# Kernel tuning notes

Hardware: AMD Instinct MI355X
Metric: run time of the kernel (lower is better)

## Reference

```python
import jax, jax.numpy as jnp
import numpy as np

BATCH = 8
HEADS = 16
Q_LEN = 1024
K_LEN = 1024
HEAD_DIM = 64


def setup_inputs() -> dict:
    key = jax.random.key(0)
    kq, kk, kv, kl = jax.random.split(key, 4)
    queries = jax.random.normal(kq, (BATCH * HEADS, Q_LEN, HEAD_DIM), dtype=jnp.float32)
    keys = jax.random.normal(kk, (BATCH * HEADS, K_LEN, HEAD_DIM), dtype=jnp.float32)
    values = jax.random.normal(kv, (BATCH * HEADS, K_LEN, HEAD_DIM), dtype=jnp.float32)
    valid_lens = jax.random.randint(kl, (BATCH,), 0, K_LEN, dtype=jnp.int64)
    return {"queries": queries, "keys": keys, "values": values, "valid_lens": valid_lens}


def reference(queries, keys, values, valid_lens):
    # queries/keys/values: [B*H, S, d]; valid_lens: [B] int
    bh, q_len, d = queries.shape
    k_len = keys.shape[1]
    b = valid_lens.shape[0]
    h = bh // b
    scale = 1.0 / float(d) ** 0.5
    # [B*H, q, k] scores
    scores = jnp.einsum("bqd,bkd->bqk", queries, keys) * scale
    # encode_mask: True where key position >= valid_len -> fill with -1e6
    mask = jnp.arange(k_len)[None, :] >= valid_lens[:, None]  # [B, k]
    scores = scores.reshape(b, h, q_len, k_len)
    scores = jnp.where(mask[:, None, None, :], jnp.float32(-1000000.0), scores)
    attn = jax.nn.softmax(scores, axis=-1)  # [B, H, q, k]
    out = jnp.einsum("bhqk,bhkd->bhqd", attn, values.reshape(b, h, k_len, d))
    return out.reshape(bh, q_len, d)
```

## Files before the change

kernel.cpp:

```cpp
#include <hip/hip_runtime.h>


#define H_PER_B 16
#define QL 1024
#define KL 1024
#define DH 64
#define KT 64
#define QW 16
#define NW 8
#define QB (QW * NW)
#define KST 72
#define VST 72
#define PST 68

typedef float  f32x4  __attribute__((ext_vector_type(4)));
typedef short  bf16x8 __attribute__((ext_vector_type(8)));
typedef short  bf16x4 __attribute__((ext_vector_type(4)));

__device__ __forceinline__ unsigned bfbits(float f) {
    unsigned u = __builtin_bit_cast(unsigned, f);
    u += 0x7FFFu + ((u >> 16) & 1u);
    return u >> 16;
}
__device__ __forceinline__ unsigned pk2(float a, float b) {
    return bfbits(a) | (bfbits(b) << 16);
}
__device__ __forceinline__ short s2bf(float f) {
    return (short)bfbits(f);
}

__global__ __launch_bounds__(512) void attn_fwd(
    const float* __restrict__ Q, const float* __restrict__ K,
    const float* __restrict__ V, const int* __restrict__ vlen_p,
    float* __restrict__ O)
{
    const int bh    = blockIdx.x;
    const int qtile = blockIdx.y;
    const int vlen  = vlen_p[bh / H_PER_B];

    const int tid  = threadIdx.x;
    const int wave = tid >> 6;
    const int lane = tid & 63;
    const int lg   = lane >> 4;
    const int lr   = lane & 15;

    const float* Qb = Q + ((size_t)bh * QL + (size_t)qtile * QB + (size_t)wave * QW) * DH;
    const float* Kb = K + (size_t)bh * KL * DH;
    const float* Vb = V + (size_t)bh * KL * DH;

    __shared__ short Ks [2][KT][KST];
    __shared__ short VsT[2][DH][VST];
    __shared__ short Ps [NW][QW][PST];

    const float QSCALE = 0.18033688011112042f;
    bf16x8 qf[2];
#pragma unroll
    for (int dc = 0; dc < 2; ++dc) {
        const float* p = Qb + (size_t)lr * DH + dc * 32 + 8 * lg;
        float4 a = *(const float4*)p;
        float4 b = *(const float4*)(p + 4);
        uint4 u;
        u.x = pk2(a.x * QSCALE, a.y * QSCALE);
        u.y = pk2(a.z * QSCALE, a.w * QSCALE);
        u.z = pk2(b.x * QSCALE, b.y * QSCALE);
        u.w = pk2(b.z * QSCALE, b.w * QSCALE);
        qf[dc] = __builtin_bit_cast(bf16x8, u);
    }

    f32x4 acc[4];
#pragma unroll
    for (int i = 0; i < 4; ++i) acc[i] = (f32x4){0.f, 0.f, 0.f, 0.f};
    float lsum[4] = {0.f, 0.f, 0.f, 0.f};

    const bool  all_masked = (vlen == 0);
    const float msel       = all_masked ? 1.0f : 0.0f;
    const int nt = all_masked ? (KL / KT) : ((vlen + KT - 1) >> 6);

    const int kr0 = tid >> 4;
    const int dc0 = (tid & 15) * 4;
    const int vd  = tid & 63;
    const int vk0 = (tid >> 6) * 8;
    const float* Vcol = Vb + vd;

    float4 ka[2];
    float  va[8];

#define LOADK(t)                                                              \
    {                                                                         \
        const float* kp = Kb + (size_t)((t) * KT) * DH;                       \
        ka[0] = *(const float4*)(kp + (size_t)kr0 * DH + dc0);                \
        ka[1] = *(const float4*)(kp + (size_t)(kr0 + 32) * DH + dc0);         \
    }
#define LOADV(t)                                                              \
    _Pragma("unroll")                                                         \
    for (int j = 0; j < 8; ++j)                                               \
        va[j] = Vcol[(size_t)((t) * KT + vk0 + j) * DH];
#define STOREKV(b)                                                            \
    {                                                                         \
        uint2 k0 = {pk2(ka[0].x, ka[0].y), pk2(ka[0].z, ka[0].w)};            \
        uint2 k1 = {pk2(ka[1].x, ka[1].y), pk2(ka[1].z, ka[1].w)};            \
        *(bf16x4*)&Ks[b][kr0][dc0]      = __builtin_bit_cast(bf16x4, k0);     \
        *(bf16x4*)&Ks[b][kr0 + 32][dc0] = __builtin_bit_cast(bf16x4, k1);     \
        uint4 vv = {pk2(va[0], va[1]), pk2(va[2], va[3]),                     \
                    pk2(va[4], va[5]), pk2(va[6], va[7])};                    \
        *(bf16x8*)&VsT[b][vd][vk0] = __builtin_bit_cast(bf16x8, vv);          \
    }

    LOADK(0); LOADV(0); STOREKV(0);

    for (int t = 0; t < nt; ++t) {
        const int buf = t & 1;
        __syncthreads();

        if (t + 1 < nt) { LOADK(t + 1); LOADV(t + 1); }
        const int kt0 = t * KT;

#pragma unroll
        for (int kh = 0; kh < 4; ++kh) {
            f32x4 c = (f32x4){0.f, 0.f, 0.f, 0.f};
#pragma unroll
            for (int dc = 0; dc < 2; ++dc) {
                bf16x8 kf = *(const bf16x8*)&Ks[buf][kh * 16 + lr][dc * 32 + 8 * lg];
                c = __builtin_amdgcn_mfma_f32_16x16x32_bf16(qf[dc], kf, c, 0, 0, 0);
            }
            const int  kpos   = kt0 + kh * 16 + lr;
            const bool masked = (kpos >= vlen);
#pragma unroll
            for (int r = 0; r < 4; ++r) {
                float e = __builtin_amdgcn_exp2f(c[r]);
                float p = masked ? msel : e;
                lsum[r] += p;
                Ps[wave][lg * 4 + r][kh * 16 + lr] = s2bf(p);
            }
        }

#pragma unroll
        for (int u = 0; u < 2; ++u) {
            bf16x4 plo = *(const bf16x4*)&Ps[wave][lr][u * 32 + 8 * lg];
            bf16x4 phi = *(const bf16x4*)&Ps[wave][lr][u * 32 + 8 * lg + 4];
            bf16x8 pf;
#pragma unroll
            for (int j = 0; j < 4; ++j) { pf[j] = plo[j]; pf[4 + j] = phi[j]; }
#pragma unroll
            for (int dt = 0; dt < 4; ++dt) {
                bf16x8 vf = *(const bf16x8*)&VsT[buf][dt * 16 + lr][u * 32 + 8 * lg];
                acc[dt] = __builtin_amdgcn_mfma_f32_16x16x32_bf16(pf, vf, acc[dt], 0, 0, 0);
            }
        }

        if (t + 1 < nt) STOREKV((t + 1) & 1);
    }

    float inv[4];
#pragma unroll
    for (int r = 0; r < 4; ++r) {
        float sum = lsum[r];
#pragma unroll
        for (int off = 1; off < 16; off <<= 1)
            sum += __shfl_xor(sum, off, 64);
        inv[r] = 1.0f / sum;
    }

    float* Ob = O + ((size_t)bh * QL + (size_t)qtile * QB + (size_t)wave * QW) * DH;
#pragma unroll
    for (int r = 0; r < 4; ++r)
#pragma unroll
        for (int dt = 0; dt < 4; ++dt)
            Ob[(size_t)(lg * 4 + r) * DH + dt * 16 + lr] = acc[dt][r] * inv[r];
}

extern "C" void kernel_launch(void* const* d_in, const int* in_sizes, int n_in,
                              void* d_out, int out_size, void* d_ws, size_t ws_size,
                              hipStream_t stream) {
    (void)in_sizes; (void)n_in; (void)d_ws; (void)ws_size; (void)out_size;
    const float* Q    = (const float*)d_in[0];
    const float* K    = (const float*)d_in[1];
    const float* V    = (const float*)d_in[2];
    const int*   vlen = (const int*)d_in[3];
    float*       O    = (float*)d_out;

    dim3 grid(128, QL / QB);
    dim3 block(512);
    attn_fwd<<<grid, block, 0, stream>>>(Q, K, V, vlen, O);
}
```

Before: 168.5 us.

## Keep P in registers via transposed QK MFMA and ds_bpermute shuffles

The QK^T MFMA operands are swapped so each lane holds scores for one query across 4 consecutive keys. The probabilities are packed to bf16 in registers and rearranged into the PV MFMA A-operand layout with ds_bpermute, instead of going through the shared-memory Ps buffer. This removes the per-tile LDS stores and reads of P and cuts shared-memory use. Row sums are now kept per lane and reduced across lane groups at the end. The grid is also flattened to 1D so the 8 q-tiles of one head are adjacent block IDs, which should improve K/V L2 reuse.

Measured after the change: 166.8 us. About the same (-1.0%).

```diff
diff --git a/kernel.cpp b/kernel.cpp
--- a/kernel.cpp
+++ b/kernel.cpp
@@ -11,7 +11,6 @@
 #define QB (QW * NW)
 #define KST 72
 #define VST 72
-#define PST 68
 
 typedef float  f32x4  __attribute__((ext_vector_type(4)));
 typedef short  bf16x8 __attribute__((ext_vector_type(8)));
@@ -25,17 +24,15 @@
 __device__ __forceinline__ unsigned pk2(float a, float b) {
     return bfbits(a) | (bfbits(b) << 16);
 }
-__device__ __forceinline__ short s2bf(float f) {
-    return (short)bfbits(f);
-}
 
 __global__ __launch_bounds__(512) void attn_fwd(
     const float* __restrict__ Q, const float* __restrict__ K,
     const float* __restrict__ V, const int* __restrict__ vlen_p,
     float* __restrict__ O)
 {
-    const int bh    = blockIdx.x;
-    const int qtile = blockIdx.y;
+    const int id    = blockIdx.x;
+    const int qtile = id & 7;
+    const int bh    = id >> 3;
     const int vlen  = vlen_p[bh / H_PER_B];
 
     const int tid  = threadIdx.x;
@@ -50,7 +47,6 @@
 
     __shared__ short Ks [2][KT][KST];
     __shared__ short VsT[2][DH][VST];
-    __shared__ short Ps [NW][QW][PST];
 
     const float QSCALE = 0.18033688011112042f;
     bf16x8 qf[2];
@@ -70,7 +66,7 @@
     f32x4 acc[4];
 #pragma unroll
     for (int i = 0; i < 4; ++i) acc[i] = (f32x4){0.f, 0.f, 0.f, 0.f};
-    float lsum[4] = {0.f, 0.f, 0.f, 0.f};
+    float lsum = 0.f;
 
     const bool  all_masked = (vlen == 0);
     const float msel       = all_masked ? 1.0f : 0.0f;
@@ -106,6 +102,10 @@
         *(bf16x8*)&VsT[b][vd][vk0] = __builtin_bit_cast(bf16x8, vv);          \
     }
 
+    const int addr0 = (((lane & 16) << 1) | (lane & 15)) << 2;
+    const int addr1 = addr0 + 64;
+    const bool selhi = (lane & 32) != 0;
+
     LOADK(0); LOADV(0); STOREKV(0);
 
     for (int t = 0; t < nt; ++t) {
@@ -115,32 +115,45 @@
         if (t + 1 < nt) { LOADK(t + 1); LOADV(t + 1); }
         const int kt0 = t * KT;
 
+        unsigned d0[4], d1[4];
 #pragma unroll
         for (int kh = 0; kh < 4; ++kh) {
             f32x4 c = (f32x4){0.f, 0.f, 0.f, 0.f};
 #pragma unroll
             for (int dc = 0; dc < 2; ++dc) {
                 bf16x8 kf = *(const bf16x8*)&Ks[buf][kh * 16 + lr][dc * 32 + 8 * lg];
-                c = __builtin_amdgcn_mfma_f32_16x16x32_bf16(qf[dc], kf, c, 0, 0, 0);
+                c = __builtin_amdgcn_mfma_f32_16x16x32_bf16(kf, qf[dc], c, 0, 0, 0);
             }
-            const int  kpos   = kt0 + kh * 16 + lr;
-            const bool masked = (kpos >= vlen);
+            const int kbase = kt0 + kh * 16 + 4 * lg;
+            float p[4];
 #pragma unroll
             for (int r = 0; r < 4; ++r) {
                 float e = __builtin_amdgcn_exp2f(c[r]);
-                float p = masked ? msel : e;
-                lsum[r] += p;
-                Ps[wave][lg * 4 + r][kh * 16 + lr] = s2bf(p);
+                p[r] = (kbase + r >= vlen) ? msel : e;
+                lsum += p[r];
             }
+            d0[kh] = pk2(p[0], p[1]);
+            d1[kh] = pk2(p[2], p[3]);
         }
 
 #pragma unroll
         for (int u = 0; u < 2; ++u) {
-            bf16x4 plo = *(const bf16x4*)&Ps[wave][lr][u * 32 + 8 * lg];
-            bf16x4 phi = *(const bf16x4*)&Ps[wave][lr][u * 32 + 8 * lg + 4];
-            bf16x8 pf;
-#pragma unroll
-            for (int j = 0; j < 4; ++j) { pf[j] = plo[j]; pf[4 + j] = phi[j]; }
+            const int a0 = 2 * u, a1 = 2 * u + 1;
+            int lo, hi;
+            uint4 Dv;
+            lo = __builtin_amdgcn_ds_bpermute(addr0, (int)d0[a0]);
+            hi = __builtin_amdgcn_ds_bpermute(addr0, (int)d0[a1]);
+            Dv.x = (unsigned)(selhi ? hi : lo);
+            lo = __builtin_amdgcn_ds_bpermute(addr0, (int)d1[a0]);
+            hi = __builtin_amdgcn_ds_bpermute(addr0, (int)d1[a1]);
+            Dv.y = (unsigned)(selhi ? hi : lo);
+            lo = __builtin_amdgcn_ds_bpermute(addr1, (int)d0[a0]);
+            hi = __builtin_amdgcn_ds_bpermute(addr1, (int)d0[a1]);
+            Dv.z = (unsigned)(selhi ? hi : lo);
+            lo = __builtin_amdgcn_ds_bpermute(addr1, (int)d1[a0]);
+            hi = __builtin_amdgcn_ds_bpermute(addr1, (int)d1[a1]);
+            Dv.w = (unsigned)(selhi ? hi : lo);
+            bf16x8 pf = __builtin_bit_cast(bf16x8, Dv);
 #pragma unroll
             for (int dt = 0; dt < 4; ++dt) {
                 bf16x8 vf = *(const bf16x8*)&VsT[buf][dt * 16 + lr][u * 32 + 8 * lg];
@@ -151,14 +164,15 @@
         if (t + 1 < nt) STOREKV((t + 1) & 1);
     }
 
-    float inv[4];
+    float sum = lsum + __shfl_xor(lsum, 16, 64);
+    sum += __shfl_xor(sum, 32, 64);
+    const float inv = 1.0f / sum;
+    float invr[4];
 #pragma unroll
     for (int r = 0; r < 4; ++r) {
-        float sum = lsum[r];
-#pragma unroll
-        for (int off = 1; off < 16; off <<= 1)
-            sum += __shfl_xor(sum, off, 64);
-        inv[r] = 1.0f / sum;
+        int a = (lane & 48) + 4 * r;
+        invr[r] = __builtin_bit_cast(float,
+                    __builtin_amdgcn_ds_bpermute(a, __builtin_bit_cast(int, inv)));
     }
 
     float* Ob = O + ((size_t)bh * QL + (size_t)qtile * QB + (size_t)wave * QW) * DH;
@@ -166,7 +180,7 @@
     for (int r = 0; r < 4; ++r)
 #pragma unroll
         for (int dt = 0; dt < 4; ++dt)
-            Ob[(size_t)(lg * 4 + r) * DH + dt * 16 + lr] = acc[dt][r] * inv[r];
+            Ob[(size_t)(lg * 4 + r) * DH + dt * 16 + lr] = acc[dt][r] * invr[r];
 }
 
 extern "C" void kernel_launch(void* const* d_in, const int* in_sizes, int n_in,
@@ -179,7 +193,7 @@
     const int*   vlen = (const int*)d_in[3];
     float*       O    = (float*)d_out;
 
-    dim3 grid(128, QL / QB);
+    dim3 grid(128 * (QL / QB));
     dim3 block(512);
     attn_fwd<<<grid, block, 0, stream>>>(Q, K, V, vlen, O);
 }
```
